# Kernel tuning notes

Hardware: AMD Instinct MI355X
Metric: run time of the kernel (lower is better)

## Reference

```python
import jax, jax.numpy as jnp
import numpy as np

NUM_HEADS = 16


def rotate_half(x):
    half = x.shape[-1] // 2
    return jnp.concatenate([-x[..., half:], x[..., :half]], axis=-1)


def setup_inputs() -> dict:
    key = jax.random.key(0)
    k0, k1, k2 = jax.random.split(key, 3)
    S, DIM, H = 16384, 1280, NUM_HEADS
    D = DIM // H            # 80
    G, L = 16, 1024         # 16 images, 1024 patch tokens each (S = G*L)

    hidden_states = jax.random.normal(k0, (S, DIM), dtype=jnp.float32) * 0.02

    # RoPE tables over packed positions
    pos = jnp.arange(S, dtype=jnp.float32)
    inv_freq = 1.0 / (10000.0 ** (jnp.arange(0, D, 2, dtype=jnp.float32) / D))
    freqs = pos[:, None] * inv_freq[None, :]          # [S, D/2]
    emb = jnp.concatenate([freqs, freqs], axis=-1)    # [S, D]
    cos = jnp.cos(emb)
    sin = jnp.sin(emb)

    cu_seqlens = (jnp.arange(G + 1, dtype=jnp.int32) * L)

    w_qkv = jax.random.normal(k1, (DIM, 3 * DIM), dtype=jnp.float32) * 0.02
    b_qkv = jnp.zeros((3 * DIM,), dtype=jnp.float32)
    w_proj = jax.random.normal(k2, (DIM, DIM), dtype=jnp.float32) * 0.02
    b_proj = jnp.zeros((DIM,), dtype=jnp.float32)

    return {
        "hidden_states": hidden_states,
        "cos": cos,
        "sin": sin,
        "w_qkv": w_qkv,
        "b_qkv": b_qkv,
        "w_proj": w_proj,
        "b_proj": b_proj,
        "cu_seqlens": cu_seqlens,
    }


def reference(hidden_states, cos, sin, w_qkv, b_qkv, w_proj, b_proj, cu_seqlens):
    S, DIM = hidden_states.shape
    H = NUM_HEADS
    D = DIM // H
    G = cu_seqlens.shape[0] - 1   # equal-length segments
    L = S // G

    qkv = (hidden_states @ w_qkv + b_qkv).reshape(S, 3, H, D)
    q, k, v = qkv[:, 0], qkv[:, 1], qkv[:, 2]   # [S, H, D]

    # RoPE (computed in fp32 as in source)
    c = cos[:, None, :]
    s = sin[:, None, :]
    q = q * c + rotate_half(q) * s
    k = k * c + rotate_half(k) * s

    # Source applies head_dim**-0.5 on q AND SDPA's default head_dim**-0.5,
    # so effective scale is head_dim**-1.
    scale = 1.0 / D

    qg = q.reshape(G, L, H, D)
    kg = k.reshape(G, L, H, D)
    vg = v.reshape(G, L, H, D)

    scores = jnp.einsum('glhd,gmhd->ghlm', qg, kg) * scale  # [G,H,L,L]
    attn = jax.nn.softmax(scores, axis=-1)
    out = jnp.einsum('ghlm,gmhd->glhd', attn, vg)           # [G,L,H,D]
    out = out.reshape(S, H * D)
    return out @ w_proj + b_proj
```

## Files before the change

### kernel.cpp

```cpp
#include <hip/hip_runtime.h>
#include <cmath>

#define SEQ   16384
#define DIMV  1280
#define NH    16
#define HD    80
#define NG    16
#define GL    1024
#define LDQKV (3*DIMV)

typedef short s16x8 __attribute__((ext_vector_type(8)));
typedef float f32x4 __attribute__((ext_vector_type(4)));

__device__ __forceinline__ unsigned short f2bf(float f) {
    union { float f; unsigned int u; } v; v.f = f;
    unsigned int u = v.u;
    return (unsigned short)((u + 0x7FFFu + ((u >> 16) & 1u)) >> 16);
}
__device__ __forceinline__ float bf2f(unsigned short h) {
    union { unsigned int u; float f; } v; v.u = ((unsigned int)h) << 16;
    return v.f;
}
__device__ __forceinline__ unsigned int pack2(float a, float b) {
    return (unsigned int)f2bf(a) | ((unsigned int)f2bf(b) << 16);
}
__device__ __forceinline__ void gload_lds16(const void* g, void* l) {
    __builtin_amdgcn_global_load_lds(
        (const __attribute__((address_space(1))) unsigned int*)g,
        (__attribute__((address_space(3))) unsigned int*)l,
        16, 0, 0);
}

__global__ __launch_bounds__(256) void convert_bf16_kernel(
    const float* __restrict__ src, unsigned short* __restrict__ dst, int n)
{
    int i = (blockIdx.x * 256 + threadIdx.x) * 8;
    if (i >= n) return;
    float4 a = *(const float4*)&src[i];
    float4 b = *(const float4*)&src[i + 4];
    uint4 o;
    o.x = pack2(a.x, a.y); o.y = pack2(a.z, a.w);
    o.z = pack2(b.x, b.y); o.w = pack2(b.z, b.w);
    *(uint4*)&dst[i] = o;
}

__global__ __launch_bounds__(256) void transpose_bf16_kernel(
    const float* __restrict__ W, unsigned short* __restrict__ WT,
    int Kdim, int N)
{
    __shared__ float tile[32][33];
    const int bx = blockIdx.x * 32;
    const int by = blockIdx.y * 32;
    const int tx = threadIdx.x & 31, ty = threadIdx.x >> 5;
#pragma unroll
    for (int j = 0; j < 4; ++j)
        tile[ty + j * 8][tx] = W[(size_t)(by + ty + j * 8) * N + bx + tx];
    __syncthreads();
#pragma unroll
    for (int j = 0; j < 4; ++j)
        WT[(size_t)(bx + ty + j * 8) * Kdim + by + tx] =
            f2bf(tile[tx][ty + j * 8]);
}

__global__ __launch_bounds__(256) void vtranspose_kernel(
    const unsigned short* __restrict__ qkv, unsigned short* __restrict__ vT)
{
    __shared__ unsigned short tile[128][88];
    const int t  = threadIdx.x;
    const int l0 = blockIdx.x * 128;
    const int gh = blockIdx.y;
    const int g  = gh >> 4, h = gh & 15;

#pragma unroll
    for (int s = 0; s < 5; ++s) {
        int i = t + s * 256;
        int row = i / 10, c = i % 10;
        *(uint4*)&tile[row][c * 8] = *(const uint4*)
            &qkv[(size_t)(g * GL + l0 + row) * LDQKV + 2 * DIMV + h * HD + c * 8];
    }
    __syncthreads();

#pragma unroll
    for (int s = 0; s < 5; ++s) {
        int i = t + s * 256;
        int d = i / 16, c16 = i % 16;
        uint4 o;
        o.x = (unsigned int)tile[c16 * 8 + 0][d] | ((unsigned int)tile[c16 * 8 + 1][d] << 16);
        o.y = (unsigned int)tile[c16 * 8 + 2][d] | ((unsigned int)tile[c16 * 8 + 3][d] << 16);
        o.z = (unsigned int)tile[c16 * 8 + 4][d] | ((unsigned int)tile[c16 * 8 + 5][d] << 16);
        o.w = (unsigned int)tile[c16 * 8 + 6][d] | ((unsigned int)tile[c16 * 8 + 7][d] << 16);
        *(uint4*)&vT[((size_t)gh * HD + d) * GL + l0 + c16 * 8] = o;
    }
}

template <bool BF16_OUT>
__global__ __launch_bounds__(256) void gemm_bf16_kernel(
    const unsigned short* __restrict__ A,
    const unsigned short* __restrict__ BT,
    const float* __restrict__ bias,
    void* __restrict__ C, int ldc, int K)
{
    __shared__ unsigned short As[128 * 64];
    __shared__ unsigned short Bs[128 * 64];
    const int t    = threadIdx.x;
    const int w    = t >> 6, lane = t & 63;
    const int wr   = w >> 1, wc = w & 1;
    const int gr   = lane >> 4, c15 = lane & 15;
    const int bm   = blockIdx.y * 128, bn = blockIdx.x * 128;

    f32x4 acc[4][4];
#pragma unroll
    for (int m = 0; m < 4; ++m)
#pragma unroll
        for (int n = 0; n < 4; ++n) acc[m][n] = (f32x4){0.f, 0.f, 0.f, 0.f};

    for (int kt = 0; kt < K; kt += 64) {
#pragma unroll
        for (int i = 0; i < 4; ++i) {
            int idx = t + i * 256;
            int row = idx >> 3;
            int cb  = ((idx & 7) ^ (row & 7)) << 4;
            gload_lds16((const char*)A + ((size_t)(bm + row) * K + kt) * 2 + cb,
                        (char*)As + idx * 16);
            gload_lds16((const char*)BT + ((size_t)(bn + row) * K + kt) * 2 + cb,
                        (char*)Bs + idx * 16);
        }
        __syncthreads();

#pragma unroll
        for (int ks = 0; ks < 2; ++ks) {
            s16x8 af[4], bf_[4];
#pragma unroll
            for (int m = 0; m < 4; ++m) {
                int row = wr * 64 + m * 16 + c15;
                int col = (ks * 64 + gr * 16) ^ ((row & 7) << 4);
                af[m] = *(const s16x8*)((const char*)As + row * 128 + col);
            }
#pragma unroll
            for (int n = 0; n < 4; ++n) {
                int row = wc * 64 + n * 16 + c15;
                int col = (ks * 64 + gr * 16) ^ ((row & 7) << 4);
                bf_[n] = *(const s16x8*)((const char*)Bs + row * 128 + col);
            }
#pragma unroll
            for (int m = 0; m < 4; ++m)
#pragma unroll
                for (int n = 0; n < 4; ++n)
                    acc[m][n] = __builtin_amdgcn_mfma_f32_16x16x32_bf16(
                        af[m], bf_[n], acc[m][n], 0, 0, 0);
        }
        __syncthreads();
    }

#pragma unroll
    for (int m = 0; m < 4; ++m) {
        int row0 = bm + wr * 64 + m * 16 + gr * 4;
#pragma unroll
        for (int n = 0; n < 4; ++n) {
            int col = bn + wc * 64 + n * 16 + c15;
            float bv = bias[col];
#pragma unroll
            for (int j = 0; j < 4; ++j) {
                float v = acc[m][n][j] + bv;
                if (BF16_OUT)
                    ((unsigned short*)C)[(size_t)(row0 + j) * ldc + col] = f2bf(v);
                else
                    ((float*)C)[(size_t)(row0 + j) * ldc + col] = v;
            }
        }
    }
}

__global__ __launch_bounds__(256) void rope_bf16_kernel(
    unsigned short* __restrict__ qkv,
    const float* __restrict__ cos_t,
    const float* __restrict__ sin_t)
{
    int u = blockIdx.x * 256 + threadIdx.x;
    if (u >= SEQ * NH * 20) return;
    int s   = u / (NH * 20);
    int rem = u % (NH * 20);
    int h   = rem / 20;
    int d   = (rem % 20) * 2;

    float2 c  = *(const float2*)&cos_t[s * HD + d];
    float2 sn = *(const float2*)&sin_t[s * HD + d];
    size_t base = (size_t)s * LDQKV + h * HD + d;

#pragma unroll
    for (int part = 0; part < 2; ++part) {
        size_t b = base + part * DIMV;
        unsigned int lo = *(unsigned int*)&qkv[b];
        unsigned int hi = *(unsigned int*)&qkv[b + 40];
        float x0 = bf2f((unsigned short)lo), x1 = bf2f((unsigned short)(lo >> 16));
        float y0 = bf2f((unsigned short)hi), y1 = bf2f((unsigned short)(hi >> 16));
        *(unsigned int*)&qkv[b]      = pack2(x0 * c.x - y0 * sn.x, x1 * c.y - y1 * sn.y);
        *(unsigned int*)&qkv[b + 40] = pack2(y0 * c.x + x0 * sn.x, y1 * c.y + x1 * sn.y);
    }
}

__global__ __launch_bounds__(512) void attn_mfma_kernel(
    const unsigned short* __restrict__ qkv,
    const unsigned short* __restrict__ vT,
    unsigned short* __restrict__ ao)
{
    const int bx  = blockIdx.x;
    const int qt  = bx >> 8;
    const int ghi = bx & 255;
    const int h   = ghi & 15;
    const int g   = ghi >> 4;

    __shared__ unsigned short Ks[64][104];
    __shared__ unsigned short Vt[96][72];
    __shared__ unsigned short Pl[8][16][72];

    const int t    = threadIdx.x;
    const int w    = t >> 6;
    const int lane = t & 63;
    const int gr   = lane >> 4;
    const int c15  = lane & 15;

    const size_t qrow0 = (size_t)g * GL + (size_t)qt * 128;
    const unsigned short* kbase  = qkv + (size_t)g * GL * LDQKV + DIMV + h * HD;
    const unsigned short* vtbase = vT + (size_t)ghi * HD * GL;

    {
        int r = t >> 3, cp = t & 7;
        *(unsigned int*)&Ks[r][80 + cp * 2] = 0u;
    }
    for (int i = t; i < 16 * 36; i += 512) {
        int row = 80 + i / 36, c2 = i % 36;
        *(unsigned int*)&Vt[row][c2 * 2] = (row == 80) ? 0x3F803F80u : 0u;
    }

    const int  kA_r = t / 10,         kA_c = t % 10;
    const int  kB_r = (t + 512) / 10, kB_c = (t + 512) % 10;
    const int  vA_d = t >> 3,         vA_c = t & 7;
    const int  vB_d = 64 + (t >> 3);
    const bool two  = (t < 128);
    const size_t offKA = (size_t)kA_r * LDQKV + kA_c * 8;
    const size_t offKB = (size_t)kB_r * LDQKV + kB_c * 8;
    const size_t offVA = (size_t)vA_d * GL + vA_c * 8;
    const size_t offVB = (size_t)vB_d * GL + vA_c * 8;

    uint4 kra, krb, vra, vrb;
    kra = *(const uint4*)&kbase[offKA];
    vra = *(const uint4*)&vtbase[offVA];
    if (two) {
        krb = *(const uint4*)&kbase[offKB];
        vrb = *(const uint4*)&vtbase[offVB];
    }

    s16x8 qf[3];
    {
        const unsigned short* qp = qkv + (qrow0 + w * 16 + c15) * LDQKV + h * HD;
#pragma unroll
        for (int kk = 0; kk < 3; ++kk) {
            int d0 = kk * 32 + gr * 8;
            if (d0 < 80) qf[kk] = *(const s16x8*)&qp[d0];
            else         qf[kk] = (s16x8){0,0,0,0,0,0,0,0};
        }
    }

    f32x4 oacc[6];
#pragma unroll
    for (int nt = 0; nt < 6; ++nt) oacc[nt] = (f32x4){0.f, 0.f, 0.f, 0.f};

    const float SC = 1.0f / 80.0f;

    for (int kc = 0; kc < GL / 64; ++kc) {
        __syncthreads();

        *(uint4*)&Ks[kA_r][kA_c * 8] = kra;
        if (two) *(uint4*)&Ks[kB_r][kB_c * 8] = krb;
        *(uint4*)&Vt[vA_d][vA_c * 8] = vra;
        if (two) *(uint4*)&Vt[vB_d][vA_c * 8] = vrb;
        __syncthreads();

        if (kc + 1 < GL / 64) {
            const unsigned short* kb = kbase + (size_t)(kc + 1) * 64 * LDQKV;
            const unsigned short* vb = vtbase + (size_t)(kc + 1) * 64;
            kra = *(const uint4*)&kb[offKA];
            vra = *(const uint4*)&vb[offVA];
            if (two) {
                krb = *(const uint4*)&kb[offKB];
                vrb = *(const uint4*)&vb[offVB];
            }
        }

        f32x4 s[4];
#pragma unroll
        for (int nt = 0; nt < 4; ++nt) {
            f32x4 a = (f32x4){0.f, 0.f, 0.f, 0.f};
#pragma unroll
            for (int kk = 0; kk < 3; ++kk) {
                s16x8 kfrag = *(const s16x8*)&Ks[nt * 16 + c15][kk * 32 + gr * 8];
                a = __builtin_amdgcn_mfma_f32_16x16x32_bf16(qf[kk], kfrag, a, 0, 0, 0);
            }
            s[nt] = a;
        }

#pragma unroll
        for (int nt = 0; nt < 4; ++nt)
#pragma unroll
            for (int r = 0; r < 4; ++r)
                Pl[w][gr * 4 + r][nt * 16 + c15] = f2bf(__expf(s[nt][r] * SC));
        asm volatile("s_waitcnt lgkmcnt(0)" ::: "memory");
        __builtin_amdgcn_sched_barrier(0);
        s16x8 pa0 = *(const s16x8*)&Pl[w][c15][gr * 8];
        s16x8 pa1 = *(const s16x8*)&Pl[w][c15][32 + gr * 8];

#pragma unroll
        for (int nt = 0; nt < 6; ++nt) {
            s16x8 vf0 = *(const s16x8*)&Vt[nt * 16 + c15][gr * 8];
            s16x8 vf1 = *(const s16x8*)&Vt[nt * 16 + c15][32 + gr * 8];
            f32x4 o = oacc[nt];
            o = __builtin_amdgcn_mfma_f32_16x16x32_bf16(pa0, vf0, o, 0, 0, 0);
            o = __builtin_amdgcn_mfma_f32_16x16x32_bf16(pa1, vf1, o, 0, 0, 0);
            oacc[nt] = o;
        }
    }

    float inv[4];
#pragma unroll
    for (int r = 0; r < 4; ++r)
        inv[r] = 1.0f / __shfl(oacc[5][r], lane & 48);
    const size_t orow0 = qrow0 + w * 16;
#pragma unroll
    for (int nt = 0; nt < 5; ++nt)
#pragma unroll
        for (int r = 0; r < 4; ++r)
            ao[(orow0 + gr * 4 + r) * DIMV + h * HD + nt * 16 + c15] =
                f2bf(oacc[nt][r] * inv[r]);
}

extern "C" void kernel_launch(void* const* d_in, const int* in_sizes, int n_in,
                              void* d_out, int out_size, void* d_ws, size_t ws_size,
                              hipStream_t stream)
{
    const float* hidden = (const float*)d_in[0];
    const float* cos_t  = (const float*)d_in[1];
    const float* sin_t  = (const float*)d_in[2];
    const float* w_qkv  = (const float*)d_in[3];
    const float* b_qkv  = (const float*)d_in[4];
    const float* w_proj = (const float*)d_in[5];
    const float* b_proj = (const float*)d_in[6];

    float* out = (float*)d_out;

    char* ws = (char*)d_ws;
    unsigned short* qkv_bf = (unsigned short*)(ws);
    unsigned short* hbf    = (unsigned short*)(ws + 125829120);
    unsigned short* vT     = (unsigned short*)(ws + 125829120);
    unsigned short* ao_bf  = (unsigned short*)(ws + 167772160);
    unsigned short* wqkvT  = (unsigned short*)(ws + 209715200);
    unsigned short* wprojT = (unsigned short*)(ws + 219545600);

    {
        int n = SEQ * DIMV;
        convert_bf16_kernel<<<n / 8 / 256, 256, 0, stream>>>(hidden, hbf, n);
        transpose_bf16_kernel<<<dim3(3 * DIMV / 32, DIMV / 32), 256, 0, stream>>>(
            w_qkv, wqkvT, DIMV, 3 * DIMV);
        transpose_bf16_kernel<<<dim3(DIMV / 32, DIMV / 32), 256, 0, stream>>>(
            w_proj, wprojT, DIMV, DIMV);
    }
    gemm_bf16_kernel<true><<<dim3(3 * DIMV / 128, SEQ / 128), 256, 0, stream>>>(
        hbf, wqkvT, b_qkv, qkv_bf, 3 * DIMV, DIMV);
    {
        int n = SEQ * NH * 20;
        rope_bf16_kernel<<<n / 256, 256, 0, stream>>>(qkv_bf, cos_t, sin_t);
    }
    vtranspose_kernel<<<dim3(GL / 128, NG * NH), 256, 0, stream>>>(qkv_bf, vT);
    attn_mfma_kernel<<<dim3(NG * NH * (GL / 128)), 512, 0, stream>>>(
        qkv_bf, vT, ao_bf);
    gemm_bf16_kernel<false><<<dim3(DIMV / 128, SEQ / 128), 256, 0, stream>>>(
        ao_bf, wprojT, b_proj, out, DIMV, DIMV);
}
```

Baseline: 675.0 us.

## Replace GEMM with 256x256 double-buffered pipelined kernel using XCD-aware block swizzle

```diff
diff --git a/kernel.cpp b/kernel.cpp
--- a/kernel.cpp
+++ b/kernel.cpp
@@ -94,70 +94,127 @@
 }
 
 template <bool BF16_OUT>
-__global__ __launch_bounds__(256) void gemm_bf16_kernel(
+__global__ __launch_bounds__(512, 2) void gemm256_kernel(
     const unsigned short* __restrict__ A,
     const unsigned short* __restrict__ BT,
     const float* __restrict__ bias,
     void* __restrict__ C, int ldc, int K)
 {
-    __shared__ unsigned short As[128 * 64];
-    __shared__ unsigned short Bs[128 * 64];
+    __shared__ unsigned short As0[256 * 64], Bs0[256 * 64];
+    __shared__ unsigned short As1[256 * 64], Bs1[256 * 64];
+
     const int t    = threadIdx.x;
     const int w    = t >> 6, lane = t & 63;
-    const int wr   = w >> 1, wc = w & 1;
+    const int wm   = w >> 2, wn = w & 3;
     const int gr   = lane >> 4, c15 = lane & 15;
-    const int bm   = blockIdx.y * 128, bn = blockIdx.x * 128;
-
-    f32x4 acc[4][4];
-#pragma unroll
-    for (int m = 0; m < 4; ++m)
+
+    const int dd  = blockIdx.y * gridDim.x + blockIdx.x;
+    const int cpx = (gridDim.x * gridDim.y) >> 3;
+    const int sw  = (dd & 7) * cpx + (dd >> 3);
+    const int bn  = (sw / gridDim.y) * 256;
+    const int bm  = (sw % gridDim.y) * 256;
+
+    const unsigned short* Ab = A  + (size_t)bm * K;
+    const unsigned short* Bb = BT + (size_t)bn * K;
+    const int NT = K >> 6;
+
+    size_t soff[2]; int dstoff[2];
+#pragma unroll
+    for (int i = 0; i < 2; ++i) {
+        int idx = t + i * 512, r = idx >> 3, blk = idx & 7;
+        int cb  = blk ^ (r & 7);
+        soff[i]   = ((size_t)r * K + cb * 8) * 2;
+        dstoff[i] = idx * 16;
+    }
+    auto stage = [&](const unsigned short* src, unsigned short* ldsb,
+                     int kt, int hh) {
+#pragma unroll
+        for (int i = 0; i < 2; ++i)
+            gload_lds16((const char*)src + soff[i]
+                            + (size_t)hh * ((size_t)128 * K * 2)
+                            + (size_t)kt * 128,
+                        (char*)ldsb + hh * 16384 + dstoff[i]);
+    };
+
+    f32x4 acc[8][4];
+#pragma unroll
+    for (int m = 0; m < 8; ++m)
 #pragma unroll
         for (int n = 0; n < 4; ++n) acc[m][n] = (f32x4){0.f, 0.f, 0.f, 0.f};
 
-    for (int kt = 0; kt < K; kt += 64) {
-#pragma unroll
-        for (int i = 0; i < 4; ++i) {
-            int idx = t + i * 256;
-            int row = idx >> 3;
-            int cb  = ((idx & 7) ^ (row & 7)) << 4;
-            gload_lds16((const char*)A + ((size_t)(bm + row) * K + kt) * 2 + cb,
-                        (char*)As + idx * 16);
-            gload_lds16((const char*)BT + ((size_t)(bn + row) * K + kt) * 2 + cb,
-                        (char*)Bs + idx * 16);
-        }
-        __syncthreads();
-
-#pragma unroll
-        for (int ks = 0; ks < 2; ++ks) {
-            s16x8 af[4], bf_[4];
-#pragma unroll
-            for (int m = 0; m < 4; ++m) {
-                int row = wr * 64 + m * 16 + c15;
-                int col = (ks * 64 + gr * 16) ^ ((row & 7) << 4);
-                af[m] = *(const s16x8*)((const char*)As + row * 128 + col);
+    stage(Ab, As0, 0, 0); stage(Ab, As0, 0, 1);
+    stage(Bb, Bs0, 0, 0); stage(Bb, Bs0, 0, 1);
+    if (NT > 1) {
+        stage(Bb, Bs1, 1, 0); stage(Bb, Bs1, 1, 1);
+        asm volatile("s_waitcnt vmcnt(4)" ::: "memory");
+    } else {
+        asm volatile("s_waitcnt vmcnt(0)" ::: "memory");
+    }
+    __builtin_amdgcn_s_barrier();
+
+    int cur = 0;
+    for (int kt = 0; kt < NT; ++kt) {
+        const unsigned short* Ac = cur ? As1 : As0;
+        const unsigned short* Bc = cur ? Bs1 : Bs0;
+        unsigned short* An  = cur ? As0 : As1;
+        unsigned short* Bcw = cur ? Bs1 : Bs0;
+
+        s16x8 bf[4][2];
+#pragma unroll
+        for (int p = 0; p < 4; ++p) {
+            if (p == 0) {
+#pragma unroll
+                for (int n = 0; n < 4; ++n)
+#pragma unroll
+                    for (int k = 0; k < 2; ++k) {
+                        int row = wn * 64 + n * 16 + c15;
+                        bf[n][k] = *(const s16x8*)((const char*)Bc + row * 128
+                                       + ((k * 64 + gr * 16) ^ ((row & 7) << 4)));
+                    }
             }
-#pragma unroll
-            for (int n = 0; n < 4; ++n) {
-                int row = wc * 64 + n * 16 + c15;
-                int col = (ks * 64 + gr * 16) ^ ((row & 7) << 4);
-                bf_[n] = *(const s16x8*)((const char*)Bs + row * 128 + col);
-            }
-#pragma unroll
-            for (int m = 0; m < 4; ++m)
+            s16x8 af[2][2];
+#pragma unroll
+            for (int mi = 0; mi < 2; ++mi)
+#pragma unroll
+                for (int k = 0; k < 2; ++k) {
+                    int row = wm * 128 + p * 32 + mi * 16 + c15;
+                    af[mi][k] = *(const s16x8*)((const char*)Ac + row * 128
+                                    + ((k * 64 + gr * 16) ^ ((row & 7) << 4)));
+                }
+            if (p == 0 && kt + 1 < NT) stage(Ab, An, kt + 1, 0);
+            if (p == 1 && kt + 1 < NT) stage(Ab, An, kt + 1, 1);
+            if (p == 2 && kt + 2 < NT) stage(Bb, Bcw, kt + 2, 0);
+            if (p == 3 && kt + 2 < NT) stage(Bb, Bcw, kt + 2, 1);
+
+            __builtin_amdgcn_s_barrier();
+            asm volatile("s_waitcnt lgkmcnt(0)" ::: "memory");
+            __builtin_amdgcn_sched_barrier(0);
+            __builtin_amdgcn_s_setprio(1);
+#pragma unroll
+            for (int mi = 0; mi < 2; ++mi)
 #pragma unroll
                 for (int n = 0; n < 4; ++n)
-                    acc[m][n] = __builtin_amdgcn_mfma_f32_16x16x32_bf16(
-                        af[m], bf_[n], acc[m][n], 0, 0, 0);
-        }
-        __syncthreads();
-    }
-
-#pragma unroll
-    for (int m = 0; m < 4; ++m) {
-        int row0 = bm + wr * 64 + m * 16 + gr * 4;
+#pragma unroll
+                    for (int k = 0; k < 2; ++k)
+                        acc[p * 2 + mi][n] = __builtin_amdgcn_mfma_f32_16x16x32_bf16(
+                            af[mi][k], bf[n][k], acc[p * 2 + mi][n], 0, 0, 0);
+            __builtin_amdgcn_s_setprio(0);
+            if (p < 3) __builtin_amdgcn_s_barrier();
+        }
+        if (kt + 1 < NT) {
+            if (kt + 2 < NT) asm volatile("s_waitcnt vmcnt(4)" ::: "memory");
+            else             asm volatile("s_waitcnt vmcnt(0)" ::: "memory");
+        }
+        __builtin_amdgcn_s_barrier();
+        cur ^= 1;
+    }
+
+#pragma unroll
+    for (int m = 0; m < 8; ++m) {
+        int row0 = bm + wm * 128 + m * 16 + gr * 4;
 #pragma unroll
         for (int n = 0; n < 4; ++n) {
-            int col = bn + wc * 64 + n * 16 + c15;
+            int col = bn + wn * 64 + n * 16 + c15;
             float bv = bias[col];
 #pragma unroll
             for (int j = 0; j < 4; ++j) {
@@ -364,7 +421,7 @@
         transpose_bf16_kernel<<<dim3(DIMV / 32, DIMV / 32), 256, 0, stream>>>(
             w_proj, wprojT, DIMV, DIMV);
     }
-    gemm_bf16_kernel<true><<<dim3(3 * DIMV / 128, SEQ / 128), 256, 0, stream>>>(
+    gemm256_kernel<true><<<dim3(3 * DIMV / 256, SEQ / 256), 512, 0, stream>>>(
         hbf, wqkvT, b_qkv, qkv_bf, 3 * DIMV, DIMV);
     {
         int n = SEQ * NH * 20;
@@ -373,6 +430,6 @@
     vtranspose_kernel<<<dim3(GL / 128, NG * NH), 256, 0, stream>>>(qkv_bf, vT);
     attn_mfma_kernel<<<dim3(NG * NH * (GL / 128)), 512, 0, stream>>>(
         qkv_bf, vT, ao_bf);
-    gemm_bf16_kernel<false><<<dim3(DIMV / 128, SEQ / 128), 256, 0, stream>>>(
+    gemm256_kernel<false><<<dim3(DIMV / 256, SEQ / 256), 512, 0, stream>>>(
         ao_bf, wprojT, b_proj, out, DIMV, DIMV);
 }
```

Result: faster. 651.2 us (-3.5%).
